# Optimization experiments

Measured on AMD Instinct MI355X. Metric: run time of the kernel, lower is better.

## Reference

```python
import jax, jax.numpy as jnp
import numpy as np

BETA = 0.9
THRESHOLD = 1.0

B, T, I, H, O = 64, 512, 256, 512, 256


def setup_inputs() -> dict:
    key = jax.random.key(0)
    ks = jax.random.split(key, 10)
    s_in = 1.0 / np.sqrt(I)
    s_h = 1.0 / np.sqrt(H)
    return {
        "x": jax.random.normal(ks[0], (B, T, I), dtype=jnp.float32),
        "W_in": jax.random.uniform(ks[1], (H, I), jnp.float32, -s_in, s_in),
        "b_in": jax.random.uniform(ks[2], (H,), jnp.float32, -s_in, s_in),
        "W_ih": jax.random.uniform(ks[3], (H, H), jnp.float32, -s_h, s_h),
        "b_ih": jax.random.uniform(ks[4], (H,), jnp.float32, -s_h, s_h),
        "W_hh": jax.random.uniform(ks[5], (H, H), jnp.float32, -s_h, s_h),
        "b_hh": jax.random.uniform(ks[6], (H,), jnp.float32, -s_h, s_h),
        "W_out": jax.random.uniform(ks[7], (O, H), jnp.float32, -s_h, s_h),
        "b_out": jax.random.uniform(ks[8], (O,), jnp.float32, -s_h, s_h),
        "temporal_attention": jax.random.normal(ks[9], (T, O), dtype=jnp.float32),
    }


def _lif(mem, cur):
    # LIF with 'subtract' reset: new_mem*(1-s) + s*(new_mem-thr) == new_mem - s*thr
    new_mem = BETA * mem + cur
    spike = (new_mem > THRESHOLD).astype(new_mem.dtype)
    return new_mem - spike * THRESHOLD, spike


def reference(x, W_in, b_in, W_ih, b_ih, W_hh, b_hh, W_out, b_out, temporal_attention):
    dtype = x.dtype
    batch, time_steps, _ = x.shape
    hidden = W_in.shape[0]

    # Input projection for all time steps at once: (B,T,H) -> scan over T.
    input_proj = jnp.einsum('bti,hi->tbh', x, W_in) + b_in  # (T,B,H)

    mem0 = jnp.zeros((batch, hidden), dtype=dtype)
    _, hidden_spikes = jax.lax.scan(_lif, mem0, input_proj)  # (T,B,H)

    # Recurrent layer: input->hidden projection precomputed; hidden->hidden uses
    # carried membrane potential (as in the torch module).
    in_proj = jnp.einsum('tbh,gh->tbg', hidden_spikes, W_ih) + b_ih  # (T,B,H)

    def rec_step(mem, ip):
        total = ip + mem @ W_hh.T + b_hh
        return _lif(mem, total)

    _, temporal_spikes = jax.lax.scan(rec_step, mem0, in_proj)  # (T,B,H)

    out_proj = jnp.einsum('tbh,oh->tbo', temporal_spikes, W_out) + b_out  # (T,B,O)

    attn = jax.nn.softmax(temporal_attention[:time_steps], axis=0)  # (T,O)
    attended = jnp.einsum('tbo,to->bo', out_proj, attn)  # (B,O)

    # Final LIF from zero membrane: new_mem = attended; spike = (attended > thr)
    final_spikes = (attended > THRESHOLD).astype(dtype)
    return final_spikes
```

## Files before the change

kernel.cpp:

```cpp
#include <hip/hip_runtime.h>
#include <hip/hip_bf16.h>
#include <cstdint>


#define T_STEPS 512
#define BATCH 64
#define HID 512
#define IN_DIM 256
#define OUT_DIM 256
#define BETA 0.9f
#define THR 1.0f
#define SENT 0x7FC00000u

typedef __attribute__((ext_vector_type(8))) short short8;
typedef __attribute__((ext_vector_type(4))) float float4v;
typedef unsigned short ushort_t;

__global__ __launch_bounds__(256) void k_fill_nan(uint32_t* __restrict__ P) {
  const int idx = blockIdx.x * 256 + threadIdx.x;
  uint4 s = make_uint4(SENT, SENT, SENT, SENT);
  uint4* p4 = (uint4*)P;
  for (int i = idx; i < (32768 * 512) / 4; i += 65536) p4[i] = s;
}

__global__ __launch_bounds__(256) void k_split(const float* __restrict__ src,
                                               ushort_t* __restrict__ hi,
                                               ushort_t* __restrict__ lo, int n) {
  int i = blockIdx.x * 256 + threadIdx.x;
  const int stride = gridDim.x * 256;
  for (; i < n; i += stride) {
    float v = src[i];
    uint32_t u = __float_as_uint(v);
    uint32_t rh = u + 0x7FFFu + ((u >> 16) & 1u);
    ushort_t h = (ushort_t)(rh >> 16);
    float hf = __uint_as_float(((uint32_t)h) << 16);
    float l = v - hf;
    uint32_t ul = __float_as_uint(l);
    uint32_t rl = ul + 0x7FFFu + ((ul >> 16) & 1u);
    hi[i] = h;
    lo[i] = (ushort_t)(rl >> 16);
  }
}

__global__ __launch_bounds__(256) void k_softmax_t(
    const float* __restrict__ TA, float* __restrict__ attn) {
  __shared__ float redm[8][32];
  __shared__ float reds[8][32];
  const int ol = threadIdx.x & 31;
  const int tg = threadIdx.x >> 5;
  const int o = blockIdx.x * 32 + ol;
  float mx = -1e30f;
  for (int i = 0; i < 64; ++i) {
    float v = TA[(size_t)(tg * 64 + i) * OUT_DIM + o];
    mx = fmaxf(mx, v);
  }
  redm[tg][ol] = mx;
  __syncthreads();
  float m = redm[0][ol];
#pragma unroll
  for (int j = 1; j < 8; ++j) m = fmaxf(m, redm[j][ol]);
  float s = 0.f;
  for (int i = 0; i < 64; ++i) {
    float v = TA[(size_t)(tg * 64 + i) * OUT_DIM + o];
    s += __expf(v - m);
  }
  reds[tg][ol] = s;
  __syncthreads();
  float tot = 0.f;
#pragma unroll
  for (int j = 0; j < 8; ++j) tot += reds[j][ol];
  const float inv = 1.0f / tot;
  for (int i = 0; i < 64; ++i) {
    int t = tg * 64 + i;
    float v = TA[(size_t)t * OUT_DIM + o];
    attn[(size_t)t * OUT_DIM + o] = __expf(v - m) * inv;
  }
}

__global__ __launch_bounds__(256) void k_gemm_split3(
    const ushort_t* __restrict__ Ahi, const ushort_t* __restrict__ Alo,
    const ushort_t* __restrict__ Bhi, const ushort_t* __restrict__ Blo,
    const float* __restrict__ bias, float* __restrict__ C,
    int M, int N, int K) {
  __shared__ ushort_t At[2][128 * 40];
  __shared__ ushort_t Bt[2][128 * 40];
  const int tid = threadIdx.x;
  const int row0 = blockIdx.x * 128, col0 = blockIdx.y * 128;
  const int w = tid >> 6, lane = tid & 63;
  const int wm = (w >> 1) * 64, wn = (w & 1) * 64;
  const int l15 = lane & 15, quad = lane >> 4;
  float4v acc[4][4];
#pragma unroll
  for (int i = 0; i < 4; ++i)
#pragma unroll
    for (int j = 0; j < 4; ++j) acc[i][j] = (float4v){0.f, 0.f, 0.f, 0.f};

  for (int k0 = 0; k0 < K; k0 += 32) {
#pragma unroll
    for (int it = 0; it < 2; ++it) {
      int idx = it * 256 + tid;
      int r = idx >> 2;
      int c8 = (idx & 3) << 3;
      *(uint4*)(&At[0][r * 40 + c8]) =
          *(const uint4*)(&Ahi[(size_t)(row0 + r) * K + k0 + c8]);
      *(uint4*)(&At[1][r * 40 + c8]) =
          *(const uint4*)(&Alo[(size_t)(row0 + r) * K + k0 + c8]);
      *(uint4*)(&Bt[0][r * 40 + c8]) =
          *(const uint4*)(&Bhi[(size_t)(col0 + r) * K + k0 + c8]);
      *(uint4*)(&Bt[1][r * 40 + c8]) =
          *(const uint4*)(&Blo[(size_t)(col0 + r) * K + k0 + c8]);
    }
    __syncthreads();
    short8 ah[4], al[4], bh[4], bl[4];
    const int koff = quad * 8;
#pragma unroll
    for (int i = 0; i < 4; ++i) {
      ah[i] = *(const short8*)(&At[0][(wm + i * 16 + l15) * 40 + koff]);
      al[i] = *(const short8*)(&At[1][(wm + i * 16 + l15) * 40 + koff]);
      bh[i] = *(const short8*)(&Bt[0][(wn + i * 16 + l15) * 40 + koff]);
      bl[i] = *(const short8*)(&Bt[1][(wn + i * 16 + l15) * 40 + koff]);
    }
#pragma unroll
    for (int i = 0; i < 4; ++i)
#pragma unroll
      for (int j = 0; j < 4; ++j) {
        acc[i][j] = __builtin_amdgcn_mfma_f32_16x16x32_bf16(ah[i], bh[j], acc[i][j], 0, 0, 0);
        acc[i][j] = __builtin_amdgcn_mfma_f32_16x16x32_bf16(ah[i], bl[j], acc[i][j], 0, 0, 0);
        acc[i][j] = __builtin_amdgcn_mfma_f32_16x16x32_bf16(al[i], bh[j], acc[i][j], 0, 0, 0);
      }
    __syncthreads();
  }
#pragma unroll
  for (int j = 0; j < 4; ++j) {
    const int col = col0 + wn + j * 16 + l15;
    const float bv = bias ? bias[col] : 0.f;
#pragma unroll
    for (int i = 0; i < 4; ++i) {
#pragma unroll
      for (int r = 0; r < 4; ++r) {
        int row = row0 + wm + i * 16 + quad * 4 + r;
        C[(size_t)row * N + col] = acc[i][j][r] + bv;
      }
    }
  }
}

__global__ __launch_bounds__(256) void k_gemm_spike2(
    const float* __restrict__ A, const ushort_t* __restrict__ Bhi,
    const ushort_t* __restrict__ Blo, const float* __restrict__ bias,
    float* __restrict__ C, int M, int N, int K) {
  __shared__ ushort_t At[128 * 72];
  __shared__ ushort_t Bt[2][128 * 72];
  const int tid = threadIdx.x;
  const int row0 = blockIdx.x * 128, col0 = blockIdx.y * 128;
  const int w = tid >> 6, lane = tid & 63;
  const int wm = (w >> 1) * 64, wn = (w & 1) * 64;
  const int l15 = lane & 15, quad = lane >> 4;
  float4v acc[4][4];
#pragma unroll
  for (int i = 0; i < 4; ++i)
#pragma unroll
    for (int j = 0; j < 4; ++j) acc[i][j] = (float4v){0.f, 0.f, 0.f, 0.f};

  for (int k0 = 0; k0 < K; k0 += 64) {
#pragma unroll
    for (int it = 0; it < 4; ++it) {
      int idx = it * 256 + tid;
      int r = idx >> 3;
      int c8 = (idx & 7) << 3;
      uint4 pa = *(const uint4*)(&A[(size_t)(row0 + r) * K + k0 + c8]);
      uint4 pb = *(const uint4*)(&A[(size_t)(row0 + r) * K + k0 + c8 + 4]);
      uint4 st;
      st.x = (pa.x >> 16) | (pa.y & 0xFFFF0000u);
      st.y = (pa.z >> 16) | (pa.w & 0xFFFF0000u);
      st.z = (pb.x >> 16) | (pb.y & 0xFFFF0000u);
      st.w = (pb.z >> 16) | (pb.w & 0xFFFF0000u);
      *(uint4*)(&At[r * 72 + c8]) = st;
      *(uint4*)(&Bt[0][r * 72 + c8]) =
          *(const uint4*)(&Bhi[(size_t)(col0 + r) * K + k0 + c8]);
      *(uint4*)(&Bt[1][r * 72 + c8]) =
          *(const uint4*)(&Blo[(size_t)(col0 + r) * K + k0 + c8]);
    }
    __syncthreads();
#pragma unroll
    for (int ks = 0; ks < 2; ++ks) {
      short8 a[4], bh[4], bl[4];
      const int koff = ks * 32 + quad * 8;
#pragma unroll
      for (int i = 0; i < 4; ++i) {
        a[i] = *(const short8*)(&At[(wm + i * 16 + l15) * 72 + koff]);
        bh[i] = *(const short8*)(&Bt[0][(wn + i * 16 + l15) * 72 + koff]);
        bl[i] = *(const short8*)(&Bt[1][(wn + i * 16 + l15) * 72 + koff]);
      }
#pragma unroll
      for (int i = 0; i < 4; ++i)
#pragma unroll
        for (int j = 0; j < 4; ++j) {
          acc[i][j] = __builtin_amdgcn_mfma_f32_16x16x32_bf16(a[i], bh[j], acc[i][j], 0, 0, 0);
          acc[i][j] = __builtin_amdgcn_mfma_f32_16x16x32_bf16(a[i], bl[j], acc[i][j], 0, 0, 0);
        }
    }
    __syncthreads();
  }
#pragma unroll
  for (int j = 0; j < 4; ++j) {
    const int col = col0 + wn + j * 16 + l15;
    const float bv = bias ? bias[col] : 0.f;
#pragma unroll
    for (int i = 0; i < 4; ++i) {
#pragma unroll
      for (int r = 0; r < 4; ++r) {
        int row = row0 + wm + i * 16 + quad * 4 + r;
        C[(size_t)row * N + col] = acc[i][j][r] + bv;
      }
    }
  }
}

__global__ __launch_bounds__(256) void k_lif1(float* __restrict__ p) {
  const int id = blockIdx.x * 256 + threadIdx.x;
  const size_t base = (size_t)(id >> 9) * (T_STEPS * HID) + (id & 511);
  float mem = 0.f;
  for (int t0 = 0; t0 < T_STEPS; t0 += 8) {
    float v[8];
#pragma unroll
    for (int j = 0; j < 8; ++j) v[j] = p[base + (size_t)(t0 + j) * HID];
#pragma unroll
    for (int j = 0; j < 8; ++j) {
      float nm = BETA * mem + v[j];
      float sp = nm > THR ? 1.0f : 0.0f;
      p[base + (size_t)(t0 + j) * HID] = sp;
      mem = nm - sp;
    }
  }
}

__global__ __launch_bounds__(512, 2) void k_recurrent_cp(
    const float* __restrict__ W, const float* __restrict__ b_hh,
    float* __restrict__ rp, float* __restrict__ P) {
  const int tid = threadIdx.x;
  const int grp = blockIdx.x >> 3;
  const int j = blockIdx.x & 7;
  const int seg = tid >> 6;
  const int gl = tid & 63;
  const int g0 = j << 6;

  __shared__ float memLDS[2][HID];
  __shared__ float scratch[8][2][64];

  for (int i = tid; i < 2 * HID; i += 512) ((float*)memLDS)[i] = 0.f;

  float Wreg[64];
  {
    const float* wrow = W + (size_t)(g0 + gl) * HID + (seg << 6);
#pragma unroll
    for (int k4 = 0; k4 < 16; ++k4) {
      float4 w4 = *(const float4*)(wrow + 4 * k4);
      Wreg[4 * k4 + 0] = w4.x; Wreg[4 * k4 + 1] = w4.y;
      Wreg[4 * k4 + 2] = w4.z; Wreg[4 * k4 + 3] = w4.w;
    }
  }

  const int ob = tid >> 6;
  const int ogl = tid & 63;
  const int og = g0 + ogl;
  const size_t rp_base = (size_t)(grp * 2 + ob) * (T_STEPS * HID) + og;
  float bhh_v = 0.f;
  if (tid < 128) bhh_v = b_hh[og];

  const int rg = (tid < g0) ? tid : tid + 64;

  const uint32_t* Pu = (const uint32_t*)P;
  float* Pf = P;

  __syncthreads();

  for (int t = 0; t < T_STEPS; ++t) {
    float ip_v = 0.f;
    if (tid < 128) ip_v = rp[rp_base + (size_t)t * HID];

    if (t > 0 && tid < 448) {
      const size_t slot = ((size_t)(t - 1) * 32 + grp) * 1024;
      uint32_t u0 = __hip_atomic_load(Pu + slot + rg, __ATOMIC_RELAXED,
                                      __HIP_MEMORY_SCOPE_AGENT);
      uint32_t u1 = __hip_atomic_load(Pu + slot + 512 + rg, __ATOMIC_RELAXED,
                                      __HIP_MEMORY_SCOPE_AGENT);
      while (u0 == SENT || u1 == SENT) {
        __builtin_amdgcn_s_sleep(1);
        if (u0 == SENT)
          u0 = __hip_atomic_load(Pu + slot + rg, __ATOMIC_RELAXED,
                                 __HIP_MEMORY_SCOPE_AGENT);
        if (u1 == SENT)
          u1 = __hip_atomic_load(Pu + slot + 512 + rg, __ATOMIC_RELAXED,
                                 __HIP_MEMORY_SCOPE_AGENT);
      }
      memLDS[0][rg] = __uint_as_float(u0);
      memLDS[1][rg] = __uint_as_float(u1);
    }
    __syncthreads();

    float p0a = 0.f, p0b = 0.f, p1a = 0.f, p1b = 0.f;
    {
      const float4* m0 = (const float4*)&memLDS[0][seg << 6];
      const float4* m1 = (const float4*)&memLDS[1][seg << 6];
#pragma unroll
      for (int k4 = 0; k4 < 16; ++k4) {
        float4 a = m0[k4];
        float4 b = m1[k4];
        p0a = fmaf(Wreg[4 * k4 + 0], a.x, p0a);
        p0b = fmaf(Wreg[4 * k4 + 1], a.y, p0b);
        p0a = fmaf(Wreg[4 * k4 + 2], a.z, p0a);
        p0b = fmaf(Wreg[4 * k4 + 3], a.w, p0b);
        p1a = fmaf(Wreg[4 * k4 + 0], b.x, p1a);
        p1b = fmaf(Wreg[4 * k4 + 1], b.y, p1b);
        p1a = fmaf(Wreg[4 * k4 + 2], b.z, p1a);
        p1b = fmaf(Wreg[4 * k4 + 3], b.w, p1b);
      }
    }
    scratch[seg][0][gl] = p0a + p0b;
    scratch[seg][1][gl] = p1a + p1b;
    __syncthreads();

    if (tid < 128) {
      float s = 0.f;
#pragma unroll
      for (int ss = 0; ss < 8; ++ss) s += scratch[ss][ob][ogl];
      const float m_old = memLDS[ob][og];
      const float nm = BETA * m_old + ip_v + s + bhh_v;
      const float sp = nm > THR ? 1.0f : 0.0f;
      rp[rp_base + (size_t)t * HID] = sp;
      const float mnew = nm - sp;
      memLDS[ob][og] = mnew;
      const size_t slot = ((size_t)t * 32 + grp) * 1024;
      __hip_atomic_store(Pf + slot + (size_t)ob * 512 + og, mnew,
                         __ATOMIC_RELAXED, __HIP_MEMORY_SCOPE_AGENT);
    }
  }
}

__global__ __launch_bounds__(256) void k_attend(
    const float* __restrict__ op, const float* __restrict__ attn,
    const float* __restrict__ b_out, float* __restrict__ out) {
  const int b = blockIdx.x;
  const int o = threadIdx.x;
  float s = b_out[o];
  const float* opb = op + (size_t)b * T_STEPS * OUT_DIM + o;
  for (int t0 = 0; t0 < T_STEPS; t0 += 8) {
    float av[8], pv[8];
#pragma unroll
    for (int j = 0; j < 8; ++j) {
      av[j] = attn[(size_t)(t0 + j) * OUT_DIM + o];
      pv[j] = opb[(size_t)(t0 + j) * OUT_DIM];
    }
#pragma unroll
    for (int j = 0; j < 8; ++j) s = fmaf(av[j], pv[j], s);
  }
  out[b * OUT_DIM + o] = s > THR ? 1.0f : 0.0f;
}

extern "C" void kernel_launch(void* const* d_in, const int* in_sizes, int n_in,
                              void* d_out, int out_size, void* d_ws, size_t ws_size,
                              hipStream_t stream) {
  (void)in_sizes; (void)n_in; (void)out_size; (void)ws_size;
  const float* x     = (const float*)d_in[0];
  const float* W_in  = (const float*)d_in[1];
  const float* b_in  = (const float*)d_in[2];
  const float* W_ih  = (const float*)d_in[3];
  const float* b_ih  = (const float*)d_in[4];
  const float* W_hh  = (const float*)d_in[5];
  const float* b_hh  = (const float*)d_in[6];
  const float* W_out = (const float*)d_in[7];
  const float* b_out = (const float*)d_in[8];
  const float* TA    = (const float*)d_in[9];

  float* ws = (float*)d_ws;
  float* proj  = ws;
  float* rproj = proj + (size_t)32768 * 512;
  float* attn  = rproj + (size_t)32768 * 512;
  ushort_t* wih_hi = (ushort_t*)(attn + 512 * 256);
  ushort_t* wih_lo = wih_hi + 512 * 512;
  ushort_t* win_hi = wih_lo + 512 * 512;
  ushort_t* win_lo = win_hi + 512 * 256;
  ushort_t* wout_hi = win_lo + 512 * 256;
  ushort_t* wout_lo = wout_hi + 256 * 512;
  ushort_t* x_hi = (ushort_t*)rproj;
  ushort_t* x_lo = x_hi + (size_t)32768 * 256;
  float* P = proj;
  float* out_proj = proj;

  k_softmax_t<<<8, 256, 0, stream>>>(TA, attn);
  k_split<<<4096, 256, 0, stream>>>(x, x_hi, x_lo, 32768 * 256);
  k_split<<<512, 256, 0, stream>>>(W_in, win_hi, win_lo, 512 * 256);
  k_split<<<512, 256, 0, stream>>>(W_ih, wih_hi, wih_lo, 512 * 512);
  k_split<<<512, 256, 0, stream>>>(W_out, wout_hi, wout_lo, 256 * 512);

  k_gemm_split3<<<dim3(256, 4), 256, 0, stream>>>(
      x_hi, x_lo, win_hi, win_lo, b_in, proj, 32768, 512, 256);
  k_lif1<<<128, 256, 0, stream>>>(proj);
  k_gemm_spike2<<<dim3(256, 4), 256, 0, stream>>>(
      proj, wih_hi, wih_lo, b_ih, rproj, 32768, 512, 512);
  k_fill_nan<<<256, 256, 0, stream>>>((uint32_t*)P);
  k_recurrent_cp<<<256, 512, 0, stream>>>(W_hh, b_hh, rproj, P);
  k_gemm_spike2<<<dim3(256, 2), 256, 0, stream>>>(
      rproj, wout_hi, wout_lo, nullptr, out_proj, 32768, 256, 512);
  k_attend<<<64, 256, 0, stream>>>(out_proj, attn, b_out, (float*)d_out);
}
```

Before: 1.082 ms.

## Replace NaN-sentinel exchange with versioned ring buffer and XCD-local fast polling

The recurrent kernel's cross-block membrane exchange no longer uses a full T-sized buffer pre-filled with NaN sentinels. It now uses a 4-slot ring of (value, timestep) pairs, which removes the large fill kernel and most of the exchange memory traffic. Block indexing is remapped so the 8 blocks of a batch group are strided across the grid. Each block reads its XCC_ID, and when all 8 blocks of a group share an XCD it polls a non-coherent sc0 copy for lower-latency handoff, falling back to agent-scope atomics otherwise. The ring's correctness depends on no producer running more than 3 steps ahead, and both the XCD-uniformity handshake and the sc0 visibility assumption are hardware-specific risks.

```diff
diff --git a/kernel.cpp b/kernel.cpp
--- a/kernel.cpp
+++ b/kernel.cpp
@@ -10,17 +10,40 @@
 #define OUT_DIM 256
 #define BETA 0.9f
 #define THR 1.0f
-#define SENT 0x7FC00000u
+#define TABSENT 0xFFFFFFFFu
+#define SPIN_LIMIT 24
 
 typedef __attribute__((ext_vector_type(8))) short short8;
 typedef __attribute__((ext_vector_type(4))) float float4v;
+typedef __attribute__((ext_vector_type(2))) unsigned int uint2v;
 typedef unsigned short ushort_t;
 
-__global__ __launch_bounds__(256) void k_fill_nan(uint32_t* __restrict__ P) {
-  const int idx = blockIdx.x * 256 + threadIdx.x;
-  uint4 s = make_uint4(SENT, SENT, SENT, SENT);
-  uint4* p4 = (uint4*)P;
-  for (int i = idx; i < (32768 * 512) / 4; i += 65536) p4[i] = s;
+static __device__ __forceinline__ float poll_val(const uint2v* prim,
+                                                 const unsigned long long* bkp,
+                                                 uint32_t want, bool uniform) {
+  if (uniform) {
+    for (int s = 0; s < SPIN_LIMIT; ++s) {
+      uint2v u;
+      asm volatile(
+          "global_load_dwordx2 %0, %1, off sc0\n\t"
+          "s_waitcnt vmcnt(0)"
+          : "=v"(u)
+          : "v"(prim)
+          : "memory");
+      if (u.y == want) return __uint_as_float(u.x);
+      __builtin_amdgcn_s_sleep(1);
+    }
+  }
+  for (;;) {
+    unsigned long long v = __hip_atomic_load(bkp, __ATOMIC_RELAXED,
+                                             __HIP_MEMORY_SCOPE_AGENT);
+    if ((uint32_t)(v >> 32) == want) return __uint_as_float((uint32_t)v);
+    __builtin_amdgcn_s_sleep(1);
+  }
+}
+
+__global__ __launch_bounds__(256) void k_fill_tab(uint32_t* __restrict__ tab) {
+  tab[threadIdx.x] = TABSENT;
 }
 
 __global__ __launch_bounds__(256) void k_split(const float* __restrict__ src,
@@ -235,20 +258,38 @@
   }
 }
 
-__global__ __launch_bounds__(512, 2) void k_recurrent_cp(
+__global__ __launch_bounds__(512) void k_recurrent_ring(
     const float* __restrict__ W, const float* __restrict__ b_hh,
-    float* __restrict__ rp, float* __restrict__ P) {
+    float* __restrict__ rp, uint2v* __restrict__ Pr,
+    unsigned long long* __restrict__ Pb, uint32_t* __restrict__ xcdtab) {
   const int tid = threadIdx.x;
-  const int grp = blockIdx.x >> 3;
-  const int j = blockIdx.x & 7;
+  const int grp = blockIdx.x & 31;
+  const int j = blockIdx.x >> 5;
   const int seg = tid >> 6;
   const int gl = tid & 63;
   const int g0 = j << 6;
 
   __shared__ float memLDS[2][HID];
   __shared__ float scratch[8][2][64];
+  __shared__ uint32_t tabv[8];
 
   for (int i = tid; i < 2 * HID; i += 512) ((float*)memLDS)[i] = 0.f;
+
+  uint32_t myxcd;
+  asm volatile("s_getreg_b32 %0, hwreg(HW_REG_XCC_ID)" : "=s"(myxcd));
+  if (tid == 0)
+    __hip_atomic_store(&xcdtab[grp * 8 + j], myxcd, __ATOMIC_RELAXED,
+                       __HIP_MEMORY_SCOPE_AGENT);
+  if (tid < 8) {
+    uint32_t v = __hip_atomic_load(&xcdtab[grp * 8 + tid], __ATOMIC_RELAXED,
+                                   __HIP_MEMORY_SCOPE_AGENT);
+    while (v == TABSENT) {
+      __builtin_amdgcn_s_sleep(1);
+      v = __hip_atomic_load(&xcdtab[grp * 8 + tid], __ATOMIC_RELAXED,
+                            __HIP_MEMORY_SCOPE_AGENT);
+    }
+    tabv[tid] = v;
+  }
 
   float Wreg[64];
   {
@@ -270,32 +311,23 @@
 
   const int rg = (tid < g0) ? tid : tid + 64;
 
-  const uint32_t* Pu = (const uint32_t*)P;
-  float* Pf = P;
-
   __syncthreads();
+  const bool uniform = tabv[0] == tabv[1] && tabv[1] == tabv[2] &&
+                       tabv[2] == tabv[3] && tabv[3] == tabv[4] &&
+                       tabv[4] == tabv[5] && tabv[5] == tabv[6] &&
+                       tabv[6] == tabv[7];
 
   for (int t = 0; t < T_STEPS; ++t) {
     float ip_v = 0.f;
     if (tid < 128) ip_v = rp[rp_base + (size_t)t * HID];
 
     if (t > 0 && tid < 448) {
-      const size_t slot = ((size_t)(t - 1) * 32 + grp) * 1024;
-      uint32_t u0 = __hip_atomic_load(Pu + slot + rg, __ATOMIC_RELAXED,
-                                      __HIP_MEMORY_SCOPE_AGENT);
-      uint32_t u1 = __hip_atomic_load(Pu + slot + 512 + rg, __ATOMIC_RELAXED,
-                                      __HIP_MEMORY_SCOPE_AGENT);
-      while (u0 == SENT || u1 == SENT) {
-        __builtin_amdgcn_s_sleep(1);
-        if (u0 == SENT)
-          u0 = __hip_atomic_load(Pu + slot + rg, __ATOMIC_RELAXED,
-                                 __HIP_MEMORY_SCOPE_AGENT);
-        if (u1 == SENT)
-          u1 = __hip_atomic_load(Pu + slot + 512 + rg, __ATOMIC_RELAXED,
-                                 __HIP_MEMORY_SCOPE_AGENT);
-      }
-      memLDS[0][rg] = __uint_as_float(u0);
-      memLDS[1][rg] = __uint_as_float(u1);
+      const uint32_t want = (uint32_t)(t - 1);
+      const int slot = (t - 1) & 3;
+      const size_t i0 = ((size_t)(grp * 4 + slot) * 2 + 0) * 512 + rg;
+      const size_t i1 = i0 + 512;
+      memLDS[0][rg] = poll_val(Pr + i0, Pb + i0, want, uniform);
+      memLDS[1][rg] = poll_val(Pr + i1, Pb + i1, want, uniform);
     }
     __syncthreads();
 
@@ -331,9 +363,21 @@
       rp[rp_base + (size_t)t * HID] = sp;
       const float mnew = nm - sp;
       memLDS[ob][og] = mnew;
-      const size_t slot = ((size_t)t * 32 + grp) * 1024;
-      __hip_atomic_store(Pf + slot + (size_t)ob * 512 + og, mnew,
-                         __ATOMIC_RELAXED, __HIP_MEMORY_SCOPE_AGENT);
+
+      const int slot = t & 3;
+      const size_t idx = ((size_t)(grp * 4 + slot) * 2 + ob) * 512 + og;
+      const unsigned long long bv =
+          ((unsigned long long)(uint32_t)t << 32) | __float_as_uint(mnew);
+      __hip_atomic_store(Pb + idx, bv, __ATOMIC_RELAXED,
+                         __HIP_MEMORY_SCOPE_AGENT);
+      if (uniform) {
+        uint2v pv;
+        pv.x = __float_as_uint(mnew);
+        pv.y = (uint32_t)t;
+        asm volatile("global_store_dwordx2 %0, %1, off sc0" ::"v"(Pr + idx),
+                     "v"(pv)
+                     : "memory");
+      }
     }
   }
 }
@@ -383,9 +427,11 @@
   ushort_t* win_lo = win_hi + 512 * 256;
   ushort_t* wout_hi = win_lo + 512 * 256;
   ushort_t* wout_lo = wout_hi + 256 * 512;
+  uint32_t* xcdtab = (uint32_t*)(wout_lo + 256 * 512);
+  uint2v* Pr = (uint2v*)(xcdtab + 256);
+  unsigned long long* Pb = (unsigned long long*)(Pr + 32 * 4 * 2 * 512);
   ushort_t* x_hi = (ushort_t*)rproj;
   ushort_t* x_lo = x_hi + (size_t)32768 * 256;
-  float* P = proj;
   float* out_proj = proj;
 
   k_softmax_t<<<8, 256, 0, stream>>>(TA, attn);
@@ -399,8 +445,8 @@
   k_lif1<<<128, 256, 0, stream>>>(proj);
   k_gemm_spike2<<<dim3(256, 4), 256, 0, stream>>>(
       proj, wih_hi, wih_lo, b_ih, rproj, 32768, 512, 512);
-  k_fill_nan<<<256, 256, 0, stream>>>((uint32_t*)P);
-  k_recurrent_cp<<<256, 512, 0, stream>>>(W_hh, b_hh, rproj, P);
+  k_fill_tab<<<1, 256, 0, stream>>>(xcdtab);
+  k_recurrent_ring<<<256, 512, 0, stream>>>(W_hh, b_hh, rproj, Pr, Pb, xcdtab);
   k_gemm_spike2<<<dim3(256, 2), 256, 0, stream>>>(
       rproj, wout_hi, wout_lo, nullptr, out_proj, 32768, 256, 512);
   k_attend<<<64, 256, 0, stream>>>(out_proj, attn, b_out, (float*)d_out);
```

Measured after the change: 2.477 ms. 129% more time.

## Replace NaN-sentinel exchange buffer with tagged 4-slot ring buffer

Applied to the files above, without the earlier changes.

The recurrent kernel's cross-block membrane exchange moves from a full T-length float buffer, pre-filled with NaN sentinels, to a small 4-slot ring of 64-bit words, each carrying the step index in its upper half. This removes the large sentinel fill pass, and the exchange buffer can stay cache-resident instead of streaming through fresh memory every step. In exchange, polling uses 64-bit loads, and correctness depends on blocks never running more than the ring depth ahead of each other.

```diff
diff --git a/kernel.cpp b/kernel.cpp
--- a/kernel.cpp
+++ b/kernel.cpp
@@ -10,17 +10,15 @@
 #define OUT_DIM 256
 #define BETA 0.9f
 #define THR 1.0f
-#define SENT 0x7FC00000u
 
 typedef __attribute__((ext_vector_type(8))) short short8;
 typedef __attribute__((ext_vector_type(4))) float float4v;
 typedef unsigned short ushort_t;
 
-__global__ __launch_bounds__(256) void k_fill_nan(uint32_t* __restrict__ P) {
-  const int idx = blockIdx.x * 256 + threadIdx.x;
-  uint4 s = make_uint4(SENT, SENT, SENT, SENT);
-  uint4* p4 = (uint4*)P;
-  for (int i = idx; i < (32768 * 512) / 4; i += 65536) p4[i] = s;
+__global__ __launch_bounds__(256) void k_fill_ring(
+    unsigned long long* __restrict__ Pb) {
+  const int i = blockIdx.x * 256 + threadIdx.x;
+  Pb[i] = 0xFFFFFFFFFFFFFFFFull;
 }
 
 __global__ __launch_bounds__(256) void k_split(const float* __restrict__ src,
@@ -235,9 +233,9 @@
   }
 }
 
-__global__ __launch_bounds__(512, 2) void k_recurrent_cp(
+__global__ __launch_bounds__(512) void k_recurrent_ring(
     const float* __restrict__ W, const float* __restrict__ b_hh,
-    float* __restrict__ rp, float* __restrict__ P) {
+    float* __restrict__ rp, unsigned long long* __restrict__ Pb) {
   const int tid = threadIdx.x;
   const int grp = blockIdx.x >> 3;
   const int j = blockIdx.x & 7;
@@ -270,9 +268,6 @@
 
   const int rg = (tid < g0) ? tid : tid + 64;
 
-  const uint32_t* Pu = (const uint32_t*)P;
-  float* Pf = P;
-
   __syncthreads();
 
   for (int t = 0; t < T_STEPS; ++t) {
@@ -280,22 +275,26 @@
     if (tid < 128) ip_v = rp[rp_base + (size_t)t * HID];
 
     if (t > 0 && tid < 448) {
-      const size_t slot = ((size_t)(t - 1) * 32 + grp) * 1024;
-      uint32_t u0 = __hip_atomic_load(Pu + slot + rg, __ATOMIC_RELAXED,
-                                      __HIP_MEMORY_SCOPE_AGENT);
-      uint32_t u1 = __hip_atomic_load(Pu + slot + 512 + rg, __ATOMIC_RELAXED,
-                                      __HIP_MEMORY_SCOPE_AGENT);
-      while (u0 == SENT || u1 == SENT) {
+      const uint32_t want = (uint32_t)(t - 1);
+      const int slot = (t - 1) & 3;
+      const unsigned long long* b0 =
+          Pb + ((size_t)(grp * 4 + slot) * 2 + 0) * 512 + rg;
+      const unsigned long long* b1 = b0 + 512;
+      unsigned long long v0 = __hip_atomic_load(b0, __ATOMIC_RELAXED,
+                                                __HIP_MEMORY_SCOPE_AGENT);
+      unsigned long long v1 = __hip_atomic_load(b1, __ATOMIC_RELAXED,
+                                                __HIP_MEMORY_SCOPE_AGENT);
+      while ((uint32_t)(v0 >> 32) != want || (uint32_t)(v1 >> 32) != want) {
         __builtin_amdgcn_s_sleep(1);
-        if (u0 == SENT)
-          u0 = __hip_atomic_load(Pu + slot + rg, __ATOMIC_RELAXED,
+        if ((uint32_t)(v0 >> 32) != want)
+          v0 = __hip_atomic_load(b0, __ATOMIC_RELAXED,
                                  __HIP_MEMORY_SCOPE_AGENT);
-        if (u1 == SENT)
-          u1 = __hip_atomic_load(Pu + slot + 512 + rg, __ATOMIC_RELAXED,
+        if ((uint32_t)(v1 >> 32) != want)
+          v1 = __hip_atomic_load(b1, __ATOMIC_RELAXED,
                                  __HIP_MEMORY_SCOPE_AGENT);
       }
-      memLDS[0][rg] = __uint_as_float(u0);
-      memLDS[1][rg] = __uint_as_float(u1);
+      memLDS[0][rg] = __uint_as_float((uint32_t)v0);
+      memLDS[1][rg] = __uint_as_float((uint32_t)v1);
     }
     __syncthreads();
 
@@ -331,9 +330,12 @@
       rp[rp_base + (size_t)t * HID] = sp;
       const float mnew = nm - sp;
       memLDS[ob][og] = mnew;
-      const size_t slot = ((size_t)t * 32 + grp) * 1024;
-      __hip_atomic_store(Pf + slot + (size_t)ob * 512 + og, mnew,
-                         __ATOMIC_RELAXED, __HIP_MEMORY_SCOPE_AGENT);
+      const int slot = t & 3;
+      const size_t idx = ((size_t)(grp * 4 + slot) * 2 + ob) * 512 + og;
+      const unsigned long long bv =
+          ((unsigned long long)(uint32_t)t << 32) | __float_as_uint(mnew);
+      __hip_atomic_store(Pb + idx, bv, __ATOMIC_RELAXED,
+                         __HIP_MEMORY_SCOPE_AGENT);
     }
   }
 }
@@ -383,11 +385,13 @@
   ushort_t* win_lo = win_hi + 512 * 256;
   ushort_t* wout_hi = win_lo + 512 * 256;
   ushort_t* wout_lo = wout_hi + 256 * 512;
+  unsigned long long* Pb =
+      (unsigned long long*)(wout_lo + 256 * 512);
   ushort_t* x_hi = (ushort_t*)rproj;
   ushort_t* x_lo = x_hi + (size_t)32768 * 256;
-  float* P = proj;
   float* out_proj = proj;
 
+  k_fill_ring<<<512, 256, 0, stream>>>(Pb);
   k_softmax_t<<<8, 256, 0, stream>>>(TA, attn);
   k_split<<<4096, 256, 0, stream>>>(x, x_hi, x_lo, 32768 * 256);
   k_split<<<512, 256, 0, stream>>>(W_in, win_hi, win_lo, 512 * 256);
@@ -399,8 +403,7 @@
   k_lif1<<<128, 256, 0, stream>>>(proj);
   k_gemm_spike2<<<dim3(256, 4), 256, 0, stream>>>(
       proj, wih_hi, wih_lo, b_ih, rproj, 32768, 512, 512);
-  k_fill_nan<<<256, 256, 0, stream>>>((uint32_t*)P);
-  k_recurrent_cp<<<256, 512, 0, stream>>>(W_hh, b_hh, rproj, P);
+  k_recurrent_ring<<<256, 512, 0, stream>>>(W_hh, b_hh, rproj, Pb);
   k_gemm_spike2<<<dim3(256, 2), 256, 0, stream>>>(
       rproj, wout_hi, wout_lo, nullptr, out_proj, 32768, 256, 512);
   k_attend<<<64, 256, 0, stream>>>(out_proj, attn, b_out, (float*)d_out);
```

Result: no change. 1.096 ms (+1.3%).
